# Kernel optimization log

Hardware: AMD Instinct MI355X
Metric: run time of the kernel (lower is better)

Reference implementation:

```python
import jax, jax.numpy as jnp
import numpy as np

D = 1024
P = 4
TOP_K = 2
B = 8
LQ = 1024
LK = 1024


def setup_inputs() -> dict:
    key = jax.random.key(0)
    ks = jax.random.split(key, 16)
    s = 0.02
    inp = {
        "Q": jax.random.normal(ks[0], (B, LQ, D), jnp.float32),
        "src": jax.random.normal(ks[1], (P, B, LK, D), jnp.float32),
        # q_proj
        "Wq": jax.random.normal(ks[2], (D, D), jnp.float32) * s,
        "bq": jnp.zeros((D,), jnp.float32),
        # per-path k/v projections (stacked over paths)
        "Wk": jax.random.normal(ks[3], (P, D, D), jnp.float32) * s,
        "bk": jnp.zeros((P, D), jnp.float32),
        "Wv": jax.random.normal(ks[4], (P, D, D), jnp.float32) * s,
        "bv": jnp.zeros((P, D), jnp.float32),
        # path_score_mlp: Linear(D,D) -> ReLU -> Linear(D,P)
        "Wm1": jax.random.normal(ks[5], (D, D), jnp.float32) * s,
        "bm1": jnp.zeros((D,), jnp.float32),
        "Wm2": jax.random.normal(ks[6], (P, D), jnp.float32) * s,
        "bm2": jnp.zeros((P,), jnp.float32),
        # out_proj
        "Wo": jax.random.normal(ks[7], (D, D), jnp.float32) * s,
        "bo": jnp.zeros((D,), jnp.float32),
    }
    return inp


def reference(Q, src, Wq, bq, Wk, bk, Wv, bv, Wm1, bm1, Wm2, bm2, Wo, bo):
    # Q: [B,Lq,D], src: [P,B,Lk,D]; all Linears use torch convention y = x @ W.T + b
    d = Q.shape[-1]
    Qp = jnp.einsum("bqd,ed->bqe", Q, Wq) + bq                     # [B,Lq,D]
    K = jnp.einsum("pbkd,ped->pbke", src, Wk) + bk[:, None, None]  # [P,B,Lk,D]
    V = jnp.einsum("pbkd,ped->pbke", src, Wv) + bv[:, None, None]  # [P,B,Lk,D]
    logits = jnp.einsum("bqd,pbkd->pbqk", Qp, K) / jnp.sqrt(jnp.asarray(d, Qp.dtype))
    attn = jax.nn.softmax(logits, axis=-1)                          # [P,B,Lq,Lk]
    attn_out = jnp.einsum("pbqk,pbke->pbqe", attn, V)               # [P,B,Lq,D]

    # path gating from mean-pooled projected query
    pooled = Qp.mean(axis=1)                                        # [B,D]
    h = jax.nn.relu(pooled @ Wm1.T + bm1)
    path_logits = h @ Wm2.T + bm2                                   # [B,P]
    path_scores = jax.nn.softmax(path_logits, axis=-1)
    _, topk_idx = jax.lax.top_k(path_scores, TOP_K)                 # [B,top_k]
    mask = jax.nn.one_hot(topk_idx, P, dtype=path_scores.dtype).sum(axis=1)  # [B,P]
    sparse_w = path_scores * mask
    sparse_w = sparse_w / (sparse_w.sum(axis=1, keepdims=True) + 1e-8)

    out = jnp.einsum("pbqe,bp->bqe", attn_out, sparse_w)            # [B,Lq,D]
    return jnp.einsum("bqe,de->bqd", out, Wo) + bo
```

## Files before the change

kernel.cpp:

```cpp
#include <hip/hip_runtime.h>

#define D_  1024
#define B_  8
#define P_  4
#define LQk 1024
#define LKk 1024

typedef __attribute__((ext_vector_type(8))) short bf16x8;
typedef __attribute__((ext_vector_type(4))) float f32x4;
typedef __attribute__((ext_vector_type(8))) unsigned short ushort8v;

__device__ __forceinline__ unsigned short f2bf(float f) {
  unsigned int u = __float_as_uint(f);
  u += 0x7FFFu + ((u >> 16) & 1u);
  return (unsigned short)(u >> 16);
}

__device__ __forceinline__ void gload_lds16(const void* g, void* l) {
  __builtin_amdgcn_global_load_lds(
      (const __attribute__((address_space(1))) unsigned int*)g,
      (__attribute__((address_space(3))) unsigned int*)l, 16, 0, 0);
}

#define SBAR() do { __builtin_amdgcn_sched_barrier(0); __builtin_amdgcn_s_barrier(); __builtin_amdgcn_sched_barrier(0); } while (0)

__global__ __launch_bounds__(256) void convert_bf16_kernel(const float* __restrict__ in,
                                                           unsigned short* __restrict__ out) {
  long i = ((long)blockIdx.x * 256 + threadIdx.x) * 8;
  float4 v0 = *(const float4*)(in + i);
  float4 v1 = *(const float4*)(in + i + 4);
  ushort8v r;
  r[0] = f2bf(v0.x); r[1] = f2bf(v0.y); r[2] = f2bf(v0.z); r[3] = f2bf(v0.w);
  r[4] = f2bf(v1.x); r[5] = f2bf(v1.y); r[6] = f2bf(v1.z); r[7] = f2bf(v1.w);
  *(ushort8v*)(out + i) = r;
}

__global__ __launch_bounds__(256) void zero_kernel(float* __restrict__ p) {
  p[blockIdx.x * 256 + threadIdx.x] = 0.f;
}

__global__ __launch_bounds__(256) void qmean_kernel(const float* __restrict__ Q,
                                                    float* __restrict__ Qm) {
  int d = blockIdx.x * 256 + threadIdx.x;
  int b = blockIdx.y;
  int q0 = blockIdx.z * 64;
  const float* q = Q + ((long)b * LQk + q0) * D_ + d;
  float s = 0.f;
  #pragma unroll 8
  for (int i = 0; i < 64; ++i) s += q[(long)i * D_];
  atomicAdd(&Qm[b * D_ + d], s * (1.0f / 1024.0f));
}

template<int RELU>
__global__ __launch_bounds__(256) void matvec_kernel(const float* __restrict__ X,
                                                     const float* __restrict__ W,
                                                     const float* __restrict__ bias,
                                                     float* __restrict__ out) {
  int g = blockIdx.x * 4 + (threadIdx.x >> 6);
  int lane = threadIdx.x & 63;
  int b = g >> 10, e = g & 1023;
  const float* x = X + b * D_;
  const float* w = W + (long)e * D_;
  float s = 0.f;
  #pragma unroll
  for (int k = lane * 4; k < D_; k += 256) {
    float4 xv = *(const float4*)(x + k);
    float4 wv = *(const float4*)(w + k);
    s += xv.x * wv.x + xv.y * wv.y + xv.z * wv.z + xv.w * wv.w;
  }
  #pragma unroll
  for (int o = 32; o; o >>= 1) s += __shfl_xor(s, o, 64);
  if (lane == 0) {
    s += bias[e];
    if (RELU) s = fmaxf(s, 0.f);
    out[b * D_ + e] = s;
  }
}

__global__ __launch_bounds__(256) void gate_kernel(const float* __restrict__ h,
                                                   const float* __restrict__ Wm2,
                                                   const float* __restrict__ bm2,
                                                   int* __restrict__ sel,
                                                   float* __restrict__ wsel) {
  __shared__ float lg[B_][P_];
  int lane = threadIdx.x & 63, wid = threadIdx.x >> 6;
  #pragma unroll
  for (int i = 0; i < 8; ++i) {
    int pair = wid * 8 + i;
    int b = pair >> 2, p = pair & 3;
    const float* x = h + b * D_;
    const float* w = Wm2 + p * D_;
    float s = 0.f;
    for (int k = lane; k < D_; k += 64) s += x[k] * w[k];
    #pragma unroll
    for (int o = 32; o; o >>= 1) s += __shfl_xor(s, o, 64);
    if (lane == 0) lg[b][p] = s + bm2[p];
  }
  __syncthreads();
  if (threadIdx.x < B_) {
    int b = threadIdx.x;
    float v0 = lg[b][0], v1 = lg[b][1], v2 = lg[b][2], v3 = lg[b][3];
    float m = fmaxf(fmaxf(v0, v1), fmaxf(v2, v3));
    float e[4];
    e[0] = __expf(v0 - m); e[1] = __expf(v1 - m);
    e[2] = __expf(v2 - m); e[3] = __expf(v3 - m);
    float sum = e[0] + e[1] + e[2] + e[3];
    int p0 = 0;
    for (int p = 1; p < 4; ++p) if (e[p] > e[p0]) p0 = p;
    int p1 = -1;
    for (int p = 0; p < 4; ++p) { if (p == p0) continue; if (p1 < 0 || e[p] > e[p1]) p1 = p; }
    float s0 = e[p0] / sum, s1 = e[p1] / sum;
    float dn = s0 + s1 + 1e-8f;
    sel[b * 2] = p0; sel[b * 2 + 1] = p1;
    wsel[b * 2] = s0 / dn; wsel[b * 2 + 1] = s1 / dn;
  }
}

__global__ __launch_bounds__(256) void select_convert_kernel(const float* __restrict__ src,
                                                             const int* __restrict__ sel,
                                                             unsigned short* __restrict__ out) {
  int z = blockIdx.y; int b = z >> 1; int p = sel[z];
  const float* s = src + ((long)p * B_ + b) * (1024L * 1024);
  unsigned short* o = out + (long)z * (1024L * 1024);
  long i = ((long)blockIdx.x * 256 + threadIdx.x) * 8;
  float4 v0 = *(const float4*)(s + i);
  float4 v1 = *(const float4*)(s + i + 4);
  ushort8v r;
  r[0] = f2bf(v0.x); r[1] = f2bf(v0.y); r[2] = f2bf(v0.z); r[3] = f2bf(v0.w);
  r[4] = f2bf(v1.x); r[5] = f2bf(v1.y); r[6] = f2bf(v1.z); r[7] = f2bf(v1.w);
  *(ushort8v*)(o + i) = r;
}

__global__ __launch_bounds__(256) void softmax_kernel(const float* __restrict__ S,
                                                      unsigned short* __restrict__ P,
                                                      const float* __restrict__ wsel) {
  int z = blockIdx.y;
  int row = blockIdx.x * 4 + (threadIdx.x >> 6);
  int lane = threadIdx.x & 63;
  const float* s = S + ((long)z * LQk + row) * LKk;
  float4 v[4];
  #pragma unroll
  for (int i = 0; i < 4; ++i) v[i] = *(const float4*)(s + (lane + i * 64) * 4);
  float m = -1e30f;
  #pragma unroll
  for (int i = 0; i < 4; ++i)
    m = fmaxf(m, fmaxf(fmaxf(v[i].x, v[i].y), fmaxf(v[i].z, v[i].w)));
  #pragma unroll
  for (int o = 32; o; o >>= 1) m = fmaxf(m, __shfl_xor(m, o, 64));
  const float sc = 0.03125f;
  float sum = 0.f;
  #pragma unroll
  for (int i = 0; i < 4; ++i) {
    v[i].x = __expf((v[i].x - m) * sc);
    v[i].y = __expf((v[i].y - m) * sc);
    v[i].z = __expf((v[i].z - m) * sc);
    v[i].w = __expf((v[i].w - m) * sc);
    sum += v[i].x + v[i].y + v[i].z + v[i].w;
  }
  #pragma unroll
  for (int o = 32; o; o >>= 1) sum += __shfl_xor(sum, o, 64);
  float wf = wsel[z] / sum;
  unsigned short* p = P + ((long)z * LQk + row) * LKk;
  #pragma unroll
  for (int i = 0; i < 4; ++i) {
    ushort4 r;
    r.x = f2bf(v[i].x * wf); r.y = f2bf(v[i].y * wf);
    r.z = f2bf(v[i].z * wf); r.w = f2bf(v[i].w * wf);
    *(ushort4*)(p + (lane + i * 64) * 4) = r;
  }
}

template<int BIAS_MODE, int OUT_BF16, int SEL_MODE, int SPLITK2, int SWZ>
__global__ __launch_bounds__(512, 2) void gemm256(
    const unsigned short* __restrict__ A0, long sAz, long segA,
    const unsigned short* __restrict__ B0, long sBz, long segB,
    const float* __restrict__ bias0, long sBiasz,
    void* __restrict__ C0, long sCz,
    const int* __restrict__ sel, int K) {
  __shared__ unsigned short As[2][256 * 64];
  __shared__ unsigned short Bs[2][256 * 64];
  const int id = blockIdx.x;
  int tx, ty, z;
  if (SWZ) {
    int m = id & 7, j = id >> 3;
    int t = j & 15;
    z = (j >> 4) * 8 + m;
    tx = t & 3; ty = t >> 2;
  } else {
    tx = id & 3; ty = id >> 2; z = 0;
  }
  const long idxA = (SEL_MODE == 1) ? sel[z] : (SEL_MODE == 3 ? (z >> 1) : z);
  const long idxB = (SEL_MODE == 2) ? sel[z] : z;
  const unsigned short* A = A0 + idxA * sAz;
  const unsigned short* B = B0 + idxB * sBz;
  const float* bias = bias0;
  if (BIAS_MODE) bias = bias0 + ((SEL_MODE == 1 || SEL_MODE == 2) ? (long)sel[z] : (long)z) * sBiasz;

  const int tid = threadIdx.x, lane = tid & 63, wid = tid >> 6;
  const int wr = wid >> 2, wc = wid & 3;
  const long rowBase = (long)ty * 256, colBase = (long)tx * 256;

  const int srow = lane >> 3;
  const int sgran = ((lane & 7) ^ (lane >> 3)) * 8;
  const int aOff = (wr * 128 + (lane & 15)) * 64;
  const int bOff = (wc * 64 + (lane & 15)) * 64;
  const int gk0 = ((lane >> 4) ^ (lane & 7)) * 8;
  const int gk1 = (((lane >> 4) + 4) ^ (lane & 7)) * 8;

  const int NKT = K >> 6;
  const int T = NKT >> 1;

  f32x4 acc[8][4] = {};

#define STG(ISB, HALF, KT, BUF) do {                                                   \
    if ((KT) < NKT) {                                                                  \
      const unsigned short* gp_ = (ISB) ? B : A;                                       \
      const long seg_ = (ISB) ? segB : segA;                                           \
      const long kc_ = (SPLITK2 && (KT) >= 16) ? (seg_ + (long)((KT) - 16) * 64)       \
                                               : ((long)(KT) * 64);                    \
      const int rb_ = (HALF) * 128 + wid * 16;                                         \
      const long gr_ = ((ISB) ? colBase : rowBase) + rb_ + srow;                       \
      const unsigned short* g0_ = gp_ + gr_ * 1024 + kc_ + sgran;                      \
      unsigned short* l0_ = ((ISB) ? &Bs[BUF][0] : &As[BUF][0]) + rb_ * 64;            \
      gload_lds16(g0_, l0_);                                                           \
      gload_lds16(g0_ + 8 * 1024, l0_ + 8 * 64);                                       \
    }                                                                                  \
  } while (0)

#define LDA(BUF, GK, MF) (*(const bf16x8*)&As[BUF][aOff + (MF) * 1024 + (GK)])
#define LDB(BUF, GK, NF) (*(const bf16x8*)&Bs[BUF][bOff + (NF) * 1024 + (GK)])

#define MF16(AV, BV, NLO) do {                                                         \
    __builtin_amdgcn_s_setprio(1);                                                     \
    _Pragma("unroll")                                                                  \
    for (int mf_ = 0; mf_ < 8; ++mf_) {                                                \
      acc[mf_][NLO]     = __builtin_amdgcn_mfma_f32_16x16x32_bf16(AV[mf_], BV[NLO],    \
                                                                  acc[mf_][NLO], 0, 0, 0); \
      acc[mf_][(NLO)+1] = __builtin_amdgcn_mfma_f32_16x16x32_bf16(AV[mf_], BV[(NLO)+1],\
                                                                  acc[mf_][(NLO)+1], 0, 0, 0); \
    }                                                                                  \
    __builtin_amdgcn_s_setprio(0);                                                     \
  } while (0)

  STG(0, 0, 0, 0); STG(1, 0, 0, 0); STG(0, 1, 0, 0); STG(1, 1, 0, 0);
  STG(0, 0, 1, 1); STG(1, 0, 1, 1);
  __builtin_amdgcn_sched_barrier(0);
  asm volatile("s_waitcnt vmcnt(4)" ::: "memory");
  __builtin_amdgcn_s_barrier();
  __builtin_amdgcn_sched_barrier(0);

  for (int t = 0; t < T; ++t) {
    const int o = 2 * t + 1, n0 = 2 * t + 2, n1 = 2 * t + 3;
    bf16x8 a0[8], a1[8], b0[4], b1[4];
    #pragma unroll
    for (int i = 0; i < 8; ++i) a0[i] = LDA(0, gk0, i);
    #pragma unroll
    for (int i = 0; i < 4; ++i) b0[i] = LDB(0, gk0, i);
    STG(0, 1, o, 1);
    SBAR();
    MF16(a0, b0, 0);
    SBAR();
    #pragma unroll
    for (int i = 0; i < 8; ++i) a1[i] = LDA(0, gk1, i);
    #pragma unroll
    for (int i = 0; i < 4; ++i) b1[i] = LDB(0, gk1, i);
    STG(1, 1, o, 1);
    SBAR();
    MF16(a0, b0, 2);
    SBAR();
    STG(0, 0, n0, 0);
    SBAR();
    MF16(a1, b1, 0);
    SBAR();
    STG(1, 0, n0, 0);
    SBAR();
    MF16(a1, b1, 2);
    __builtin_amdgcn_sched_barrier(0);
    if (t == T - 1) { asm volatile("s_waitcnt vmcnt(0)" ::: "memory"); }
    else            { asm volatile("s_waitcnt vmcnt(4)" ::: "memory"); }
    __builtin_amdgcn_s_barrier();
    __builtin_amdgcn_sched_barrier(0);
    #pragma unroll
    for (int i = 0; i < 8; ++i) a0[i] = LDA(1, gk0, i);
    #pragma unroll
    for (int i = 0; i < 4; ++i) b0[i] = LDB(1, gk0, i);
    STG(0, 1, n0, 0);
    SBAR();
    MF16(a0, b0, 0);
    SBAR();
    #pragma unroll
    for (int i = 0; i < 8; ++i) a1[i] = LDA(1, gk1, i);
    #pragma unroll
    for (int i = 0; i < 4; ++i) b1[i] = LDB(1, gk1, i);
    STG(1, 1, n0, 0);
    SBAR();
    MF16(a0, b0, 2);
    SBAR();
    STG(0, 0, n1, 1);
    SBAR();
    MF16(a1, b1, 0);
    SBAR();
    STG(1, 0, n1, 1);
    SBAR();
    MF16(a1, b1, 2);
    if (t < T - 1) {
      __builtin_amdgcn_sched_barrier(0);
      asm volatile("s_waitcnt vmcnt(4)" ::: "memory");
      __builtin_amdgcn_s_barrier();
      __builtin_amdgcn_sched_barrier(0);
    }
  }
#undef STG
#undef LDA
#undef LDB
#undef MF16

  unsigned short* Cb = (unsigned short*)C0 + (long)z * sCz;
  float* Cf = (float*)C0 + (long)z * sCz;
  const long crow0 = rowBase + wr * 128;
  const long ccol0 = colBase + wc * 64;
  #pragma unroll
  for (int mf = 0; mf < 8; ++mf) {
    #pragma unroll
    for (int j = 0; j < 4; ++j) {
      const long row = crow0 + mf * 16 + (lane >> 4) * 4 + j;
      const float brow = (BIAS_MODE == 2) ? bias[row] : 0.f;
      #pragma unroll
      for (int nf = 0; nf < 4; ++nf) {
        const long col = ccol0 + nf * 16 + (lane & 15);
        float v = acc[mf][nf][j] + brow;
        if (BIAS_MODE == 1) v += bias[col];
        if (OUT_BF16) Cb[row * 1024 + col] = f2bf(v);
        else          Cf[row * 1024 + col] = v;
      }
    }
  }
}

extern "C" void kernel_launch(void* const* d_in, const int* in_sizes, int n_in,
                              void* d_out, int out_size, void* d_ws, size_t ws_size,
                              hipStream_t stream) {
  (void)in_sizes; (void)n_in; (void)out_size; (void)ws_size;
  const float* Q   = (const float*)d_in[0];
  const float* src = (const float*)d_in[1];
  const float* Wq  = (const float*)d_in[2];
  const float* bq  = (const float*)d_in[3];
  const float* Wk  = (const float*)d_in[4];
  const float* bk  = (const float*)d_in[5];
  const float* Wv  = (const float*)d_in[6];
  const float* bv  = (const float*)d_in[7];
  const float* Wm1 = (const float*)d_in[8];
  const float* bm1 = (const float*)d_in[9];
  const float* Wm2 = (const float*)d_in[10];
  const float* bm2 = (const float*)d_in[11];
  const float* Wo  = (const float*)d_in[12];
  const float* bo  = (const float*)d_in[13];
  float* out = (float*)d_out;

  char* ws = (char*)d_ws;
  const long MBb = 1024L * 1024;
  const long ME  = 1024L * 1024;
  unsigned short* Qbf   = (unsigned short*)(ws);
  unsigned short* srcbf = (unsigned short*)(ws + 16 * MBb);
  unsigned short* Wkbf  = (unsigned short*)(ws + 48 * MBb);
  unsigned short* Wvbf  = (unsigned short*)(ws + 56 * MBb);
  float*          Sbuf  = (float*)(ws);
  unsigned short* Qpbf  = (unsigned short*)(ws + 64 * MBb);
  unsigned short* Wqbf  = (unsigned short*)(ws + 80 * MBb);
  unsigned short* Wobf  = (unsigned short*)(ws + 82 * MBb);
  unsigned short* Kbf   = (unsigned short*)(ws + 84 * MBb);
  unsigned short* Vtbf  = (unsigned short*)(ws + 116 * MBb);
  unsigned short* Pbf   = (unsigned short*)(ws + 148 * MBb);
  unsigned short* AObf  = (unsigned short*)(ws + 180 * MBb);
  float* Qmean  = (float*)(ws + 196 * MBb);
  float* pooled = (float*)(ws + 196 * MBb + 32 * 1024);
  float* hbuf   = (float*)(ws + 196 * MBb + 64 * 1024);
  int*   sel    = (int*)(ws + 196 * MBb + 96 * 1024);
  float* wsel   = (float*)(ws + 196 * MBb + 96 * 1024 + 256);

  convert_bf16_kernel<<<4096, 256, 0, stream>>>(Q, Qbf);
  convert_bf16_kernel<<<512,  256, 0, stream>>>(Wq, Wqbf);
  convert_bf16_kernel<<<2048, 256, 0, stream>>>(Wk, Wkbf);
  convert_bf16_kernel<<<2048, 256, 0, stream>>>(Wv, Wvbf);
  convert_bf16_kernel<<<512,  256, 0, stream>>>(Wo, Wobf);

  zero_kernel<<<32, 256, 0, stream>>>(Qmean);
  qmean_kernel<<<dim3(4, 8, 16), 256, 0, stream>>>(Q, Qmean);
  matvec_kernel<0><<<2048, 256, 0, stream>>>(Qmean, Wq, bq, pooled);
  matvec_kernel<1><<<2048, 256, 0, stream>>>(pooled, Wm1, bm1, hbuf);
  gate_kernel<<<1, 256, 0, stream>>>(hbuf, Wm2, bm2, sel, wsel);

  select_convert_kernel<<<dim3(512, 16), 256, 0, stream>>>(src, sel, srcbf);

  gemm256<1,1,0,0,0><<<128, 512, 0, stream>>>(Qbf, 0, 0, Wqbf, 0, 0, bq, 0, Qpbf, 0, nullptr, 1024);
  gemm256<1,1,2,0,1><<<256, 512, 0, stream>>>(srcbf, ME, 0, Wkbf, ME, 0, bk, D_, Kbf, ME, sel, 1024);
  gemm256<2,1,1,0,1><<<256, 512, 0, stream>>>(Wvbf, ME, 0, srcbf, ME, 0, bv, D_, Vtbf, ME, sel, 1024);
  gemm256<0,0,3,0,1><<<256, 512, 0, stream>>>(Qpbf, ME, 0, Kbf, ME, 0, nullptr, 0, Sbuf, ME, nullptr, 1024);
  softmax_kernel<<<dim3(256, 16), 256, 0, stream>>>(Sbuf, Pbf, wsel);
  gemm256<0,1,0,1,1><<<128, 512, 0, stream>>>(Pbf, 2 * ME, ME, Vtbf, 2 * ME, ME, nullptr, 0, AObf, ME, nullptr, 2048);
  gemm256<1,0,0,0,0><<<128, 512, 0, stream>>>(AObf, 0, 0, Wobf, 0, 0, bo, 0, out, 0, nullptr, 1024);
}
```

Baseline: 621.5 us.

## Replace split-K PV GEMM with per-path GEMMs plus combine, relax sched barriers

The P·V GEMM, which previously summed both selected paths inside one K=2048 launch of 128 blocks, now runs as 256 separate K=1024 products into fp32 scratch. A new combine kernel then adds each pair and converts the sum to bf16. This doubles the blocks in flight for better CU occupancy, at the cost of an extra fp32 write and read of the intermediate. It also removes most sched_barrier fences and half the s_barriers in the GEMM main loop, giving the compiler more freedom to interleave LDS loads with MFMAs, which risks LDS races if the barriers were needed.

```diff
diff --git a/kernel.cpp b/kernel.cpp
--- a/kernel.cpp
+++ b/kernel.cpp
@@ -21,8 +21,6 @@
       (const __attribute__((address_space(1))) unsigned int*)g,
       (__attribute__((address_space(3))) unsigned int*)l, 16, 0, 0);
 }
-
-#define SBAR() do { __builtin_amdgcn_sched_barrier(0); __builtin_amdgcn_s_barrier(); __builtin_amdgcn_sched_barrier(0); } while (0)
 
 __global__ __launch_bounds__(256) void convert_bf16_kernel(const float* __restrict__ in,
                                                            unsigned short* __restrict__ out) {
@@ -170,10 +168,24 @@
   }
 }
 
-template<int BIAS_MODE, int OUT_BF16, int SEL_MODE, int SPLITK2, int SWZ>
+__global__ __launch_bounds__(256) void combine_kernel(const float* __restrict__ S,
+                                                      unsigned short* __restrict__ AO) {
+  int b = blockIdx.y;
+  long i = ((long)blockIdx.x * 256 + threadIdx.x) * 4;
+  const float* p0 = S + (long)(2 * b) * (1024L * 1024) + i;
+  const float* p1 = S + (long)(2 * b + 1) * (1024L * 1024) + i;
+  float4 v0 = *(const float4*)p0;
+  float4 v1 = *(const float4*)p1;
+  ushort4 r;
+  r.x = f2bf(v0.x + v1.x); r.y = f2bf(v0.y + v1.y);
+  r.z = f2bf(v0.z + v1.z); r.w = f2bf(v0.w + v1.w);
+  *(ushort4*)(AO + (long)b * (1024L * 1024) + i) = r;
+}
+
+template<int BIAS_MODE, int OUT_BF16, int SEL_MODE, int SWZ>
 __global__ __launch_bounds__(512, 2) void gemm256(
-    const unsigned short* __restrict__ A0, long sAz, long segA,
-    const unsigned short* __restrict__ B0, long sBz, long segB,
+    const unsigned short* __restrict__ A0, long sAz,
+    const unsigned short* __restrict__ B0, long sBz,
     const float* __restrict__ bias0, long sBiasz,
     void* __restrict__ C0, long sCz,
     const int* __restrict__ sel, int K) {
@@ -215,9 +227,7 @@
 #define STG(ISB, HALF, KT, BUF) do {                                                   \
     if ((KT) < NKT) {                                                                  \
       const unsigned short* gp_ = (ISB) ? B : A;                                       \
-      const long seg_ = (ISB) ? segB : segA;                                           \
-      const long kc_ = (SPLITK2 && (KT) >= 16) ? (seg_ + (long)((KT) - 16) * 64)       \
-                                               : ((long)(KT) * 64);                    \
+      const long kc_ = (long)(KT) * 64;                                                \
       const int rb_ = (HALF) * 128 + wid * 16;                                         \
       const long gr_ = ((ISB) ? colBase : rowBase) + rb_ + srow;                       \
       const unsigned short* g0_ = gp_ + gr_ * 1024 + kc_ + sgran;                      \
@@ -242,12 +252,12 @@
     __builtin_amdgcn_s_setprio(0);                                                     \
   } while (0)
 
+#define BAR() __builtin_amdgcn_s_barrier()
+
   STG(0, 0, 0, 0); STG(1, 0, 0, 0); STG(0, 1, 0, 0); STG(1, 1, 0, 0);
   STG(0, 0, 1, 1); STG(1, 0, 1, 1);
-  __builtin_amdgcn_sched_barrier(0);
   asm volatile("s_waitcnt vmcnt(4)" ::: "memory");
   __builtin_amdgcn_s_barrier();
-  __builtin_amdgcn_sched_barrier(0);
 
   for (int t = 0; t < T; ++t) {
     const int o = 2 * t + 1, n0 = 2 * t + 2, n1 = 2 * t + 3;
@@ -257,63 +267,56 @@
     #pragma unroll
     for (int i = 0; i < 4; ++i) b0[i] = LDB(0, gk0, i);
     STG(0, 1, o, 1);
-    SBAR();
+    BAR();
     MF16(a0, b0, 0);
-    SBAR();
     #pragma unroll
     for (int i = 0; i < 8; ++i) a1[i] = LDA(0, gk1, i);
     #pragma unroll
     for (int i = 0; i < 4; ++i) b1[i] = LDB(0, gk1, i);
     STG(1, 1, o, 1);
-    SBAR();
+    BAR();
+    __builtin_amdgcn_sched_barrier(0);
     MF16(a0, b0, 2);
-    SBAR();
     STG(0, 0, n0, 0);
-    SBAR();
+    BAR();
     MF16(a1, b1, 0);
-    SBAR();
     STG(1, 0, n0, 0);
-    SBAR();
+    BAR();
     MF16(a1, b1, 2);
-    __builtin_amdgcn_sched_barrier(0);
     if (t == T - 1) { asm volatile("s_waitcnt vmcnt(0)" ::: "memory"); }
     else            { asm volatile("s_waitcnt vmcnt(4)" ::: "memory"); }
     __builtin_amdgcn_s_barrier();
-    __builtin_amdgcn_sched_barrier(0);
     #pragma unroll
     for (int i = 0; i < 8; ++i) a0[i] = LDA(1, gk0, i);
     #pragma unroll
     for (int i = 0; i < 4; ++i) b0[i] = LDB(1, gk0, i);
     STG(0, 1, n0, 0);
-    SBAR();
+    BAR();
     MF16(a0, b0, 0);
-    SBAR();
     #pragma unroll
     for (int i = 0; i < 8; ++i) a1[i] = LDA(1, gk1, i);
     #pragma unroll
     for (int i = 0; i < 4; ++i) b1[i] = LDB(1, gk1, i);
     STG(1, 1, n0, 0);
-    SBAR();
+    BAR();
+    __builtin_amdgcn_sched_barrier(0);
     MF16(a0, b0, 2);
-    SBAR();
     STG(0, 0, n1, 1);
-    SBAR();
+    BAR();
     MF16(a1, b1, 0);
-    SBAR();
     STG(1, 0, n1, 1);
-    SBAR();
+    BAR();
     MF16(a1, b1, 2);
     if (t < T - 1) {
-      __builtin_amdgcn_sched_barrier(0);
       asm volatile("s_waitcnt vmcnt(4)" ::: "memory");
       __builtin_amdgcn_s_barrier();
-      __builtin_amdgcn_sched_barrier(0);
     }
   }
 #undef STG
 #undef LDA
 #undef LDB
 #undef MF16
+#undef BAR
 
   unsigned short* Cb = (unsigned short*)C0 + (long)z * sCz;
   float* Cf = (float*)C0 + (long)z * sCz;
@@ -392,11 +395,12 @@
 
   select_convert_kernel<<<dim3(512, 16), 256, 0, stream>>>(src, sel, srcbf);
 
-  gemm256<1,1,0,0,0><<<128, 512, 0, stream>>>(Qbf, 0, 0, Wqbf, 0, 0, bq, 0, Qpbf, 0, nullptr, 1024);
-  gemm256<1,1,2,0,1><<<256, 512, 0, stream>>>(srcbf, ME, 0, Wkbf, ME, 0, bk, D_, Kbf, ME, sel, 1024);
-  gemm256<2,1,1,0,1><<<256, 512, 0, stream>>>(Wvbf, ME, 0, srcbf, ME, 0, bv, D_, Vtbf, ME, sel, 1024);
-  gemm256<0,0,3,0,1><<<256, 512, 0, stream>>>(Qpbf, ME, 0, Kbf, ME, 0, nullptr, 0, Sbuf, ME, nullptr, 1024);
+  gemm256<1,1,0,0><<<128, 512, 0, stream>>>(Qbf, 0, Wqbf, 0, bq, 0, Qpbf, 0, nullptr, 1024);
+  gemm256<1,1,2,1><<<256, 512, 0, stream>>>(srcbf, ME, Wkbf, ME, bk, D_, Kbf, ME, sel, 1024);
+  gemm256<2,1,1,1><<<256, 512, 0, stream>>>(Wvbf, ME, srcbf, ME, bv, D_, Vtbf, ME, sel, 1024);
+  gemm256<0,0,3,1><<<256, 512, 0, stream>>>(Qpbf, ME, Kbf, ME, nullptr, 0, Sbuf, ME, nullptr, 1024);
   softmax_kernel<<<dim3(256, 16), 256, 0, stream>>>(Sbuf, Pbf, wsel);
-  gemm256<0,1,0,1,1><<<128, 512, 0, stream>>>(Pbf, 2 * ME, ME, Vtbf, 2 * ME, ME, nullptr, 0, AObf, ME, nullptr, 2048);
-  gemm256<1,0,0,0,0><<<128, 512, 0, stream>>>(AObf, 0, 0, Wobf, 0, 0, bo, 0, out, 0, nullptr, 1024);
-}
+  gemm256<0,0,0,1><<<256, 512, 0, stream>>>(Pbf, ME, Vtbf, ME, nullptr, 0, Sbuf, ME, nullptr, 1024);
+  combine_kernel<<<dim3(1024, 8), 256, 0, stream>>>(Sbuf, AObf);
+  gemm256<1,0,0,0><<<128, 512, 0, stream>>>(AObf, 0, Wobf, 0, bo, 0, out, 0, nullptr, 1024);
+}
```

Measured after the change: 583.0 us. 6.2% less time.
